# Optimization experiments

Hardware: AMD Instinct MI355X
Metric: run time of the kernel (lower is better)

Reference implementation:

```python
import jax, jax.numpy as jnp
import numpy as np

N = 262144      # number of 3D points
D = 128         # in_channels
NCLS = 20       # classes
M = 10          # num_prototype
EPS = 0.05      # sinkhorn epsilon
ITERS = 3       # sinkhorn iterations
GAMMA = 0.99    # EMA momentum
LN_EPS = 1e-5

def layer_norm(x, g, b):
    mu = jnp.mean(x, axis=-1, keepdims=True)
    v = jnp.mean((x - mu) ** 2, axis=-1, keepdims=True)
    return (x - mu) / jnp.sqrt(v + LN_EPS) * g + b

def l2n(x):
    # F.normalize(p=2, dim=-1) with eps=1e-12
    return x / jnp.clip(jnp.linalg.norm(x, axis=-1, keepdims=True), 1e-12)

def setup_inputs() -> dict:
    key = jax.random.key(0)
    k1, k2, k3 = jax.random.split(key, 3)
    return {
        "feature3d": jax.random.normal(k1, (N, D), dtype=jnp.float32),
        "gt_seg": jax.random.randint(k2, (N,), 0, NCLS, dtype=jnp.int32),
        "prototypes": jax.random.normal(k3, (NCLS, M, D), dtype=jnp.float32),
        "feat_gamma": jnp.ones((D,), jnp.float32),
        "feat_beta": jnp.zeros((D,), jnp.float32),
        "mask_gamma": jnp.ones((NCLS,), jnp.float32),
        "mask_beta": jnp.zeros((NCLS,), jnp.float32),
    }

def reference(feature3d, gt_seg, prototypes, feat_gamma, feat_beta, mask_gamma, mask_beta):
    _c = l2n(layer_norm(feature3d, feat_gamma, feat_beta))            # [N,D]
    protos = l2n(prototypes)                                          # [K,M,D]
    masks = jnp.einsum('nd,kmd->nmk', _c, protos)                     # [N,M,K]
    out_seg = layer_norm(jnp.max(masks, axis=1), mask_gamma, mask_beta)  # [N,K]

    # ---- prototype_learning ----
    pred = jnp.argmax(out_seg, axis=-1)
    correct = (gt_seg == pred).astype(_c.dtype)                       # [N]
    proto_logits = _c @ protos.reshape(-1, D).T                       # [N,K*M]

    sel = jax.nn.one_hot(gt_seg, NCLS, dtype=_c.dtype)                # [N,K]
    # masked per-class sinkhorn, vectorized across all 20 classes
    L = jnp.exp(jnp.transpose(masks, (2, 1, 0)) / EPS) * sel.T[:, None, :]  # [K,M,N]
    B = jnp.sum(sel, axis=0)                                          # [K] points per class
    s = jnp.sum(L, axis=(1, 2), keepdims=True)
    L = L / jnp.where(s > 0, s, 1.0)
    Bsafe = jnp.where(B > 0, B, 1.0)[:, None, None]
    for _ in range(ITERS):
        rs = jnp.sum(L, axis=2, keepdims=True)                        # per-prototype row sum
        L = L / (jnp.where(rs > 0, rs, 1.0) * M)
        cs = jnp.sum(L, axis=1, keepdims=True)                        # per-point col sum
        L = L / jnp.where(cs > 0, cs, 1.0) / Bsafe
    L = L * B[:, None, None]

    idx = jnp.argmax(L, axis=1)                                       # [K,N] hard assignment
    q = jax.nn.one_hot(idx, M, dtype=_c.dtype)                        # [K,N,M] (one_hot(argmax))

    w = sel.T * correct[None, :]                                      # [K,N] class-k AND correct
    m_q = q * w[:, :, None]                                           # [K,N,M]
    f = jnp.einsum('knm,nd->kmd', m_q, _c * correct[:, None])         # [K,M,D]
    ncount = jnp.sum(m_q, axis=1)                                     # [K,M]
    fn = l2n(f)
    upd = GAMMA * protos + (1.0 - GAMMA) * fn                         # momentum_update
    new_protos = l2n(jnp.where(ncount[..., None] > 0, upd, protos))   # [K,M,D]

    idx_pp = idx[gt_seg, jnp.arange(N)]                               # per-point proto index
    proto_target = (idx_pp + M * gt_seg).astype(jnp.float32)          # [N]
    return out_seg, proto_logits, proto_target, new_protos
```

## Files before the change

kernel.cpp:

```cpp
#include <hip/hip_runtime.h>
#include <hip/hip_bf16.h>

#define NPTS 262144
#define DIM  128
#define KC   20
#define MP   10
#define LNEPS 1e-5f
#define EPSI  0.05f
#define CCAP  65536

typedef _Float16 half8 __attribute__((ext_vector_type(8)));
typedef float f32x4 __attribute__((ext_vector_type(4)));

union H8U4 { half8 h; uint4 u; };

#define WS_PN     0
#define WS_PHI    25600
#define WS_PLO    39936
#define WS_F      54272
#define WS_NCOUNT 79872
#define WS_CCNT   80072
#define WS_UH     80080
#define WS_SK     80680
#define WS_BC     80700
#define WS_PSB    80720
#define WS_PR     244560
#define WS_EXPV   449360
#define WS_CIDX   3595088

#define MFMA_(b_, a_, c_) __builtin_amdgcn_mfma_f32_16x16x32_f16(b_, a_, c_, 0, 0, 0)

__device__ __forceinline__ half8 lds_h8(const uint4* p) {
    return *reinterpret_cast<const half8*>(p);
}

__device__ __forceinline__ void gload_lds16(const uint4* g, uint4* l) {
    __builtin_amdgcn_global_load_lds(
        (const __attribute__((address_space(1))) void*)(g),
        (__attribute__((address_space(3))) void*)(l), 16, 0, 0);
}

__global__ __launch_bounds__(64) void k_norm_protos(
    const float* __restrict__ pr, float* __restrict__ pn,
    _Float16* __restrict__ phi, _Float16* __restrict__ plo)
{
    int j = blockIdx.x, l = threadIdx.x;
    const int jm = j & 15;
    const int s1 = l >> 3,       swz1 = (((s1 ^ jm) << 3) | (l & 7));
    const int s2 = 8 + (l >> 3), swz2 = (((s2 ^ jm) << 3) | (l & 7));
    if (j < 200) {
        float x0 = pr[(size_t)j*128 + l], x1 = pr[(size_t)j*128 + 64 + l];
        float ss = x0*x0 + x1*x1;
        #pragma unroll
        for (int off = 32; off > 0; off >>= 1) ss += __shfl_xor(ss, off);
        float dn = fmaxf(sqrtf(ss), 1e-12f);
        float y0 = x0/dn, y1 = x1/dn;
        pn[(size_t)j*128 + l]      = y0;
        pn[(size_t)j*128 + 64 + l] = y1;
        _Float16 h0 = (_Float16)y0, h1 = (_Float16)y1;
        phi[(size_t)j*128 + swz1] = h0;
        phi[(size_t)j*128 + swz2] = h1;
        plo[(size_t)j*128 + swz1] = (_Float16)(y0 - (float)h0);
        plo[(size_t)j*128 + swz2] = (_Float16)(y1 - (float)h1);
    } else {
        phi[(size_t)j*128 + swz1] = (_Float16)0.f;  phi[(size_t)j*128 + swz2] = (_Float16)0.f;
        plo[(size_t)j*128 + swz1] = (_Float16)0.f;  plo[(size_t)j*128 + swz2] = (_Float16)0.f;
    }
}

__global__ __launch_bounds__(256, 3) void k_main(
    const float* __restrict__ feat, const int* __restrict__ gt,
    const _Float16* __restrict__ phi, const _Float16* __restrict__ plo,
    const float* __restrict__ fg, const float* __restrict__ fb,
    const float* __restrict__ mg, const float* __restrict__ mb,
    float* __restrict__ out_seg, float* __restrict__ plog,
    float* __restrict__ expv, float* __restrict__ psb,
    int* __restrict__ cidx, int* __restrict__ ccnt)
{
    __shared__ __align__(16) char ldsb[49152];
    __shared__ float sumS[64];
    __shared__ int   gtS[64];
    __shared__ float part[320];
    uint4* bbuf = (uint4*)ldsb;
    float* epi  = (float*)ldsb;

    const int t = threadIdx.x, blk = blockIdx.x;
    const int w = t >> 6, lane = t & 63;
    const int l15 = lane & 15, l4 = lane >> 4;
    const int pbase = blk * 64;

    const uint4* phi4 = (const uint4*)phi;
    const uint4* plo4 = (const uint4*)plo;

#define STAGE_B(S, BI) do { \
        const uint4* gh = phi4 + (size_t)(S)*512 + t; \
        const uint4* gl = plo4 + (size_t)(S)*512 + t; \
        uint4* dh = bbuf + (BI)*1024 + w*64; \
        uint4* dl = bbuf + (BI)*1024 + 512 + w*64; \
        gload_lds16(gh,       dh); \
        gload_lds16(gh + 256, dh + 256); \
        gload_lds16(gl,       dl); \
        gload_lds16(gl + 256, dl + 256); \
    } while (0)

    STAGE_B(0, 0);
    STAGE_B(1, 1);

    const float4* gfeat = (const float4*)feat;
    float4 A[4][2];
    {
        size_t rb = (size_t)(pbase + w*16 + l15) * 32;
        #pragma unroll
        for (int kst = 0; kst < 4; ++kst)
            #pragma unroll
            for (int h = 0; h < 2; ++h)
                A[kst][h] = gfeat[rb + kst*8 + l4*2 + h];
    }
    float4 G[4][2], Bb[4][2];
    {
        const float4* fg4 = (const float4*)fg;
        const float4* fb4 = (const float4*)fb;
        #pragma unroll
        for (int kst = 0; kst < 4; ++kst)
            #pragma unroll
            for (int h = 0; h < 2; ++h) {
                G[kst][h]  = fg4[kst*8 + l4*2 + h];
                Bb[kst][h] = fb4[kst*8 + l4*2 + h];
            }
    }

    half8 fah[4], fal[4];
    {
        float s0 = 0.f;
        #pragma unroll
        for (int kst = 0; kst < 4; ++kst)
            #pragma unroll
            for (int h = 0; h < 2; ++h) {
                float4 v = A[kst][h];
                s0 += v.x + v.y + v.z + v.w;
            }
        s0 += __shfl_xor(s0, 16); s0 += __shfl_xor(s0, 32);
        float mean = s0 * (1.f/128.f);
        float s1 = 0.f;
        #pragma unroll
        for (int kst = 0; kst < 4; ++kst)
            #pragma unroll
            for (int h = 0; h < 2; ++h) {
                float4 v = A[kst][h];
                float a = v.x-mean, b = v.y-mean, c = v.z-mean, d = v.w-mean;
                s1 += a*a + b*b + c*c + d*d;
            }
        s1 += __shfl_xor(s1, 16); s1 += __shfl_xor(s1, 32);
        float rstd = rsqrtf(s1 * (1.f/128.f) + LNEPS);
        float s2 = 0.f;
        #pragma unroll
        for (int kst = 0; kst < 4; ++kst)
            #pragma unroll
            for (int h = 0; h < 2; ++h) {
                float4 v = A[kst][h];
                float4 g = G[kst][h], bb = Bb[kst][h];
                v.x = (v.x-mean)*rstd*g.x + bb.x;
                v.y = (v.y-mean)*rstd*g.y + bb.y;
                v.z = (v.z-mean)*rstd*g.z + bb.z;
                v.w = (v.w-mean)*rstd*g.w + bb.w;
                A[kst][h] = v;
                s2 += v.x*v.x + v.y*v.y + v.z*v.z + v.w*v.w;
            }
        s2 += __shfl_xor(s2, 16); s2 += __shfl_xor(s2, 32);
        float rl2 = 1.f / fmaxf(sqrtf(s2), 1e-12f);
        #pragma unroll
        for (int kst = 0; kst < 4; ++kst) {
            float4 va = A[kst][0], vb = A[kst][1];
            va.x*=rl2; va.y*=rl2; va.z*=rl2; va.w*=rl2;
            vb.x*=rl2; vb.y*=rl2; vb.z*=rl2; vb.w*=rl2;
            H8U4 h, lo;
            h.h[0]=(_Float16)va.x; h.h[1]=(_Float16)va.y; h.h[2]=(_Float16)va.z; h.h[3]=(_Float16)va.w;
            h.h[4]=(_Float16)vb.x; h.h[5]=(_Float16)vb.y; h.h[6]=(_Float16)vb.z; h.h[7]=(_Float16)vb.w;
            lo.h[0]=(_Float16)(va.x-(float)h.h[0]); lo.h[1]=(_Float16)(va.y-(float)h.h[1]);
            lo.h[2]=(_Float16)(va.z-(float)h.h[2]); lo.h[3]=(_Float16)(va.w-(float)h.h[3]);
            lo.h[4]=(_Float16)(vb.x-(float)h.h[4]); lo.h[5]=(_Float16)(vb.y-(float)h.h[5]);
            lo.h[6]=(_Float16)(vb.z-(float)h.h[6]); lo.h[7]=(_Float16)(vb.w-(float)h.h[7]);
            fah[kst] = h.h;
            fal[kst] = lo.h;
        }
    }

    f32x4 acc[13];
    #pragma unroll
    for (int nt = 0; nt < 13; ++nt)
        acc[nt] = (f32x4){0.f,0.f,0.f,0.f};

    __syncthreads();

    #pragma unroll
    for (int s = 0; s < 7; ++s) {
        if (s < 5) STAGE_B(s + 2, (s + 2) % 3);
        const uint4* bb = bbuf + (s % 3)*1024;
        if (s < 6) {
            #pragma unroll
            for (int kst = 0; kst < 4; ++kst) {
                const int slz = (kst*4 + l4) ^ l15;
                half8 b0h = lds_h8(bb + l15*16 + slz);
                half8 b0l = lds_h8(bb + 512 + l15*16 + slz);
                half8 b1h = lds_h8(bb + (16+l15)*16 + slz);
                half8 b1l = lds_h8(bb + 512 + (16+l15)*16 + slz);
                acc[2*s]   = MFMA_(b0h, fah[kst], acc[2*s]);
                acc[2*s+1] = MFMA_(b1h, fah[kst], acc[2*s+1]);
                acc[2*s]   = MFMA_(b0h, fal[kst], acc[2*s]);
                acc[2*s+1] = MFMA_(b1h, fal[kst], acc[2*s+1]);
                acc[2*s]   = MFMA_(b0l, fah[kst], acc[2*s]);
                acc[2*s+1] = MFMA_(b1l, fah[kst], acc[2*s+1]);
                acc[2*s]   = MFMA_(b0l, fal[kst], acc[2*s]);
                acc[2*s+1] = MFMA_(b1l, fal[kst], acc[2*s+1]);
            }
        } else {
            #pragma unroll
            for (int kst = 0; kst < 4; ++kst) {
                const int slz = (kst*4 + l4) ^ l15;
                half8 b0h = lds_h8(bb + l15*16 + slz);
                half8 b0l = lds_h8(bb + 512 + l15*16 + slz);
                acc[12] = MFMA_(b0h, fah[kst], acc[12]);
                acc[12] = MFMA_(b0h, fal[kst], acc[12]);
                acc[12] = MFMA_(b0l, fah[kst], acc[12]);
                acc[12] = MFMA_(b0l, fal[kst], acc[12]);
            }
        }
        __syncthreads();
    }

    #pragma unroll 1
    for (int p = 0; p < 2; ++p) {
        if ((w >> 1) == p) {
            int row = (w & 1)*16 + l15;
            #pragma unroll
            for (int nt = 0; nt < 13; ++nt)
                if (nt < 12 || l4 < 2) {
                    float4 sv;
                    sv.x = acc[nt][0]; sv.y = acc[nt][1];
                    sv.z = acc[nt][2]; sv.w = acc[nt][3];
                    *reinterpret_cast<float4*>(&epi[row*210 + nt*16 + l4*4]) = sv;
                }
        }
        __syncthreads();
        if (t < 128) {
            const int q = t >> 2, sub = t & 3;
            const int n = pbase + p*32 + q;
            float ml[5];
            #pragma unroll
            for (int kk = 0; kk < 5; ++kk) {
                int k = sub*5 + kk;
                float mx = epi[q*210 + k*10];
                #pragma unroll
                for (int m = 1; m < 10; ++m) mx = fmaxf(mx, epi[q*210 + k*10 + m]);
                ml[kk] = mx;
            }
            float s0 = ml[0]+ml[1]+ml[2]+ml[3]+ml[4];
            s0 += __shfl_xor(s0,1); s0 += __shfl_xor(s0,2);
            float mean = s0 / 20.f;
            float s1 = 0.f;
            #pragma unroll
            for (int kk = 0; kk < 5; ++kk) { float d = ml[kk]-mean; s1 += d*d; }
            s1 += __shfl_xor(s1,1); s1 += __shfl_xor(s1,2);
            float rstd = rsqrtf(s1 / 20.f + LNEPS);
            float bv = -1e30f; int bk = 0;
            #pragma unroll
            for (int kk = 0; kk < 5; ++kk) {
                int k = sub*5 + kk;
                float y = (ml[kk]-mean)*rstd*mg[k] + mb[k];
                out_seg[(size_t)n*20 + k] = y;
                if (y > bv) { bv = y; bk = k; }
            }
            #pragma unroll
            for (int off = 1; off <= 2; off <<= 1) {
                float ov = __shfl_xor(bv, off);
                int   ok = __shfl_xor(bk, off);
                if (ov > bv || (ov == bv && ok < bk)) { bv = ov; bk = ok; }
            }
            int g = gt[n];
            if (sub == 0) {
                if (bk == g) {
                    int slot = atomicAdd(ccnt, 1);
                    if (slot < CCAP) cidx[slot] = n;
                }
                float se = 0.f;
                #pragma unroll
                for (int m = 0; m < 10; ++m) {
                    float e = expf(epi[q*210 + g*10 + m] / EPSI);
                    expv[(size_t)n*12 + m] = e;
                    se += e;
                }
                sumS[p*32 + q] = se;
                gtS[p*32 + q]  = g;
            }
        }
        __syncthreads();
    }

    if (t < 160) {
        int c = t >> 3, o = t & 7;
        float cnt = 0.f, sm = 0.f;
        for (int i = o*8; i < o*8 + 8; ++i)
            if (gtS[i] == c) { cnt += 1.f; sm += sumS[i]; }
        part[t] = cnt; part[160 + t] = sm;
    }
    __syncthreads();
    if (t < 20) {
        float cnt = 0.f, sm = 0.f;
        #pragma unroll
        for (int o = 0; o < 8; ++o) { cnt += part[t*8+o]; sm += part[160 + t*8+o]; }
        psb[(size_t)t*4096 + blk]      = cnt;
        psb[(size_t)(20+t)*4096 + blk] = sm;
    }

    #pragma unroll
    for (int nt = 0; nt < 13; ++nt)
        if (nt < 12 || l4 < 2) {
            float4 sv;
            sv.x = acc[nt][0]; sv.y = acc[nt][1];
            sv.z = acc[nt][2]; sv.w = acc[nt][3];
            *reinterpret_cast<float4*>(
                &plog[(size_t)(pbase + w*16 + l15)*200 + nt*16 + l4*4]) = sv;
        }
#undef STAGE_B
}

__global__ __launch_bounds__(256) void k_reduce_sB(
    const float* __restrict__ psb, float* __restrict__ sk, float* __restrict__ Bc)
{
    __shared__ float red[256];
    int t = threadIdx.x, rrow = blockIdx.x;
    float s = 0.f;
    #pragma unroll
    for (int i = 0; i < 16; ++i) s += psb[(size_t)rrow*4096 + i*256 + t];
    red[t] = s; __syncthreads();
    for (int off = 128; off > 0; off >>= 1) { if (t < off) red[t] += red[t+off]; __syncthreads(); }
    if (t == 0) { if (rrow < 20) Bc[rrow] = red[0]; else sk[rrow-20] = red[0]; }
}

__global__ __launch_bounds__(256) void k_row(int iter,
    const int* __restrict__ gt, const float* __restrict__ expv,
    const float* __restrict__ uh, const float* __restrict__ sk,
    const float* __restrict__ Bc, float* __restrict__ pr)
{
    __shared__ float prodS[2560];
    __shared__ int gtS[256];
    int t = threadIdx.x, b = blockIdx.x;
    int n = b*256 + t;
    int g = gt[n];
    float e[10];
    {
        const float4* e4 = (const float4*)(expv + (size_t)n*12);
        float4 ea = e4[0], eb = e4[1], ec = e4[2];
        e[0]=ea.x; e[1]=ea.y; e[2]=ea.z; e[3]=ea.w;
        e[4]=eb.x; e[5]=eb.y; e[6]=eb.z; e[7]=eb.w;
        e[8]=ec.x; e[9]=ec.y;
    }
    float skg = sk[g];
    float v = (skg > 0.f) ? 1.f/skg : 1.f;
    float B = Bc[g];
    float Bs = (B > 0.f) ? B : 1.f;
    for (int c = 1; c < iter; ++c) {
        const float* uc = uh + (c-1)*200 + g*10;
        float sc = 0.f;
        #pragma unroll
        for (int m = 0; m < 10; ++m) sc += e[m]*uc[m];
        v = (sc > 0.f) ? 1.f/(Bs*sc) : v/Bs;
    }
    #pragma unroll
    for (int m = 0; m < 10; ++m) prodS[t*10+m] = e[m]*v;
    gtS[t] = g;
    __syncthreads();
    if (t < 200) {
        int kk = t / 10, mm = t % 10;
        float acc = 0.f;
        for (int i = 0; i < 256; ++i)
            if (gtS[i] == kk) acc += prodS[i*10+mm];
        pr[(size_t)t*1024 + b] = acc;
    }
}

__global__ __launch_bounds__(256) void k_reduce_u(int iter,
    const float* __restrict__ pr, float* __restrict__ uh)
{
    __shared__ float red[256];
    int t = threadIdx.x, j = blockIdx.x;
    float s = 0.f;
    #pragma unroll
    for (int i = 0; i < 4; ++i) s += pr[(size_t)j*1024 + i*256 + t];
    red[t] = s; __syncthreads();
    for (int off = 128; off > 0; off >>= 1) { if (t < off) red[t] += red[t+off]; __syncthreads(); }
    if (t == 0) {
        float S = red[0];
        float uprev = (iter == 1) ? 1.f : uh[(iter-2)*200 + j];
        uh[(iter-1)*200 + j] = (S > 0.f) ? 1.f/(10.f*S) : uprev*0.1f;
    }
}

__global__ __launch_bounds__(256) void k_post(
    const int* __restrict__ gt, const float* __restrict__ expv,
    const float* __restrict__ u,
    const int* __restrict__ cidx, const int* __restrict__ ccnt,
    const float* __restrict__ feat, const float* __restrict__ fg,
    const float* __restrict__ fb,
    float* __restrict__ ptarget, float* __restrict__ facc,
    float* __restrict__ ncount)
{
    int t = threadIdx.x;
    {
        int n = blockIdx.x*256 + t;
        int g = gt[n];
        const float* uk = u + g*10;
        float bv = -1e30f; int idx = 0;
        #pragma unroll
        for (int m = 0; m < 10; ++m) {
            float pm = expv[(size_t)n*12 + m] * uk[m];
            if (pm > bv) { bv = pm; idx = m; }
        }
        ptarget[n] = (float)(idx + 10*g);
    }
    int wid = blockIdx.x*4 + (t >> 6);
    int lane = t & 63;
    int cnt = *ccnt; if (cnt > CCAP) cnt = CCAP;
    for (int i = wid; i < cnt; i += 4096) {
        int n = cidx[i];
        float x0 = feat[(size_t)n*128 + lane], x1 = feat[(size_t)n*128 + 64 + lane];
        float s = x0 + x1;
        #pragma unroll
        for (int off = 32; off > 0; off >>= 1) s += __shfl_xor(s, off);
        float mean = s * (1.f/128.f);
        float d0 = x0 - mean, d1 = x1 - mean;
        float s2 = d0*d0 + d1*d1;
        #pragma unroll
        for (int off = 32; off > 0; off >>= 1) s2 += __shfl_xor(s2, off);
        float rstd = rsqrtf(s2 * (1.f/128.f) + LNEPS);
        float y0 = d0*rstd*fg[lane] + fb[lane];
        float y1 = d1*rstd*fg[64+lane] + fb[64+lane];
        float s3 = y0*y0 + y1*y1;
        #pragma unroll
        for (int off = 32; off > 0; off >>= 1) s3 += __shfl_xor(s3, off);
        float rl2 = 1.f / fmaxf(sqrtf(s3), 1e-12f);
        float c0 = y0*rl2, c1 = y1*rl2;
        int g = gt[n];
        const float* uk = u + g*10;
        float bv = -1e30f; int idx = 0;
        #pragma unroll
        for (int m = 0; m < 10; ++m) {
            float pm = expv[(size_t)n*12 + m] * uk[m];
            if (pm > bv) { bv = pm; idx = m; }
        }
        float* frow = facc + (size_t)(g*10+idx)*128;
        atomicAdd(&frow[lane], c0);
        atomicAdd(&frow[64+lane], c1);
        if (lane == 0) atomicAdd(&ncount[g*10+idx], 1.f);
    }
}

__global__ __launch_bounds__(64) void k_proto_update(
    const float* __restrict__ facc, const float* __restrict__ ncount,
    const float* __restrict__ pn, float* __restrict__ outp)
{
    const float OMG = (float)(1.0 - 0.99);
    int j = blockIdx.x, l = threadIdx.x;
    float f0 = facc[(size_t)j*128+l], f1 = facc[(size_t)j*128+64+l];
    float ss = f0*f0 + f1*f1;
    #pragma unroll
    for (int off = 32; off > 0; off >>= 1) ss += __shfl_xor(ss, off);
    float fl2 = fmaxf(sqrtf(ss), 1e-12f);
    float fn0 = f0/fl2, fn1 = f1/fl2;
    float p0 = pn[(size_t)j*128+l], p1 = pn[(size_t)j*128+64+l];
    float u0 = 0.99f*p0 + OMG*fn0, u1 = 0.99f*p1 + OMG*fn1;
    bool ok = ncount[j] > 0.f;
    float s0 = ok ? u0 : p0, s1 = ok ? u1 : p1;
    float ss2 = s0*s0 + s1*s1;
    #pragma unroll
    for (int off = 32; off > 0; off >>= 1) ss2 += __shfl_xor(ss2, off);
    float l2 = fmaxf(sqrtf(ss2), 1e-12f);
    outp[(size_t)j*128+l]      = s0/l2;
    outp[(size_t)j*128+64+l]   = s1/l2;
}

extern "C" void kernel_launch(void* const* d_in, const int* in_sizes, int n_in,
                              void* d_out, int out_size, void* d_ws, size_t ws_size,
                              hipStream_t stream)
{
    const float* feat   = (const float*)d_in[0];
    const int*   gt     = (const int*)  d_in[1];
    const float* protos = (const float*)d_in[2];
    const float* fg     = (const float*)d_in[3];
    const float* fb     = (const float*)d_in[4];
    const float* mg     = (const float*)d_in[5];
    const float* mb     = (const float*)d_in[6];

    float* out      = (float*)d_out;
    float* out_seg  = out;
    float* plog     = out + (size_t)NPTS*20;
    float* ptarget  = out + (size_t)NPTS*220;
    float* newp     = out + (size_t)NPTS*221;

    float* ws   = (float*)d_ws;
    float* pn   = ws + WS_PN;
    _Float16* phi = (_Float16*)(ws + WS_PHI);
    _Float16* plo = (_Float16*)(ws + WS_PLO);
    float* facc = ws + WS_F;
    float* ncnt = ws + WS_NCOUNT;
    int*   ccnt = (int*)(ws + WS_CCNT);
    float* uh   = ws + WS_UH;
    float* sk   = ws + WS_SK;
    float* Bc   = ws + WS_BC;
    float* psb  = ws + WS_PSB;
    float* pr   = ws + WS_PR;
    float* expv = ws + WS_EXPV;
    int*   cidx = (int*)(ws + WS_CIDX);

    hipMemsetAsync(facc, 0, (25600 + 200 + 8)*sizeof(float), stream);
    hipLaunchKernelGGL(k_norm_protos, dim3(224), dim3(64), 0, stream, protos, pn, phi, plo);
    hipLaunchKernelGGL(k_main, dim3(4096), dim3(256), 0, stream,
                       feat, gt, phi, plo, fg, fb, mg, mb, out_seg, plog, expv, psb,
                       cidx, ccnt);
    hipLaunchKernelGGL(k_reduce_sB, dim3(40), dim3(256), 0, stream, psb, sk, Bc);
    for (int it = 1; it <= 3; ++it) {
        hipLaunchKernelGGL(k_row, dim3(1024), dim3(256), 0, stream, it, gt, expv, uh, sk, Bc, pr);
        hipLaunchKernelGGL(k_reduce_u, dim3(200), dim3(256), 0, stream, it, pr, uh);
    }
    hipLaunchKernelGGL(k_post, dim3(1024), dim3(256), 0, stream,
                       gt, expv, uh + 400, cidx, ccnt, feat, fg, fb, ptarget, facc, ncnt);
    hipLaunchKernelGGL(k_proto_update, dim3(200), dim3(64), 0, stream, facc, ncnt, pn, newp);
}
```

Measured before the change: 270.2 us.

## Coalesce k_main output stores via LDS and fuse Sinkhorn reductions into row kernels

```diff
diff --git a/kernel.cpp b/kernel.cpp
--- a/kernel.cpp
+++ b/kernel.cpp
@@ -28,6 +28,8 @@
 #define WS_EXPV   449360
 #define WS_CIDX   3595088
 
+#define EPIT 212
+
 #define MFMA_(b_, a_, c_) __builtin_amdgcn_mfma_f32_16x16x32_f16(b_, a_, c_, 0, 0, 0)
 
 __device__ __forceinline__ half8 lds_h8(const uint4* p) {
@@ -83,6 +85,8 @@
     __shared__ float part[320];
     uint4* bbuf = (uint4*)ldsb;
     float* epi  = (float*)ldsb;
+    float* osg  = (float*)(ldsb + 28672);
+    float* exs  = (float*)(ldsb + 31232);
 
     const int t = threadIdx.x, blk = blockIdx.x;
     const int w = t >> 6, lane = t & 63;
@@ -238,10 +242,22 @@
                     float4 sv;
                     sv.x = acc[nt][0]; sv.y = acc[nt][1];
                     sv.z = acc[nt][2]; sv.w = acc[nt][3];
-                    *reinterpret_cast<float4*>(&epi[row*210 + nt*16 + l4*4]) = sv;
+                    *reinterpret_cast<float4*>(&epi[row*EPIT + nt*16 + l4*4]) = sv;
                 }
         }
         __syncthreads();
+        {
+            float* pdst = plog + (size_t)(pbase + p*32)*200;
+            #pragma unroll
+            for (int it = 0; it < 7; ++it) {
+                int f = it*256 + t;
+                if (f < 1600) {
+                    int row = f / 50, c4 = f - row*50;
+                    float4 v = *reinterpret_cast<const float4*>(&epi[row*EPIT + c4*4]);
+                    *reinterpret_cast<float4*>(&pdst[(size_t)f*4]) = v;
+                }
+            }
+        }
         if (t < 128) {
             const int q = t >> 2, sub = t & 3;
             const int n = pbase + p*32 + q;
@@ -249,9 +265,9 @@
             #pragma unroll
             for (int kk = 0; kk < 5; ++kk) {
                 int k = sub*5 + kk;
-                float mx = epi[q*210 + k*10];
+                float mx = epi[q*EPIT + k*10];
                 #pragma unroll
-                for (int m = 1; m < 10; ++m) mx = fmaxf(mx, epi[q*210 + k*10 + m]);
+                for (int m = 1; m < 10; ++m) mx = fmaxf(mx, epi[q*EPIT + k*10 + m]);
                 ml[kk] = mx;
             }
             float s0 = ml[0]+ml[1]+ml[2]+ml[3]+ml[4];
@@ -267,7 +283,7 @@
             for (int kk = 0; kk < 5; ++kk) {
                 int k = sub*5 + kk;
                 float y = (ml[kk]-mean)*rstd*mg[k] + mb[k];
-                out_seg[(size_t)n*20 + k] = y;
+                osg[q*20 + k] = y;
                 if (y > bv) { bv = y; bk = k; }
             }
             #pragma unroll
@@ -285,14 +301,23 @@
                 float se = 0.f;
                 #pragma unroll
                 for (int m = 0; m < 10; ++m) {
-                    float e = expf(epi[q*210 + g*10 + m] / EPSI);
-                    expv[(size_t)n*12 + m] = e;
+                    float e = expf(epi[q*EPIT + g*10 + m] / EPSI);
+                    exs[q*12 + m] = e;
                     se += e;
                 }
+                exs[q*12 + 10] = 0.f;
+                exs[q*12 + 11] = 0.f;
                 sumS[p*32 + q] = se;
                 gtS[p*32 + q]  = g;
             }
         }
+        __syncthreads();
+        if (t < 160)
+            *reinterpret_cast<float4*>(&out_seg[(size_t)(pbase + p*32)*20 + t*4])
+                = *reinterpret_cast<const float4*>(&osg[t*4]);
+        else if (t < 256 && (t - 160) < 96)
+            *reinterpret_cast<float4*>(&expv[(size_t)(pbase + p*32)*12 + (t-160)*4])
+                = *reinterpret_cast<const float4*>(&exs[(t-160)*4]);
         __syncthreads();
     }
 
@@ -311,16 +336,6 @@
         psb[(size_t)t*4096 + blk]      = cnt;
         psb[(size_t)(20+t)*4096 + blk] = sm;
     }
-
-    #pragma unroll
-    for (int nt = 0; nt < 13; ++nt)
-        if (nt < 12 || l4 < 2) {
-            float4 sv;
-            sv.x = acc[nt][0]; sv.y = acc[nt][1];
-            sv.z = acc[nt][2]; sv.w = acc[nt][3];
-            *reinterpret_cast<float4*>(
-                &plog[(size_t)(pbase + w*16 + l15)*200 + nt*16 + l4*4]) = sv;
-        }
 #undef STAGE_B
 }
 
@@ -339,77 +354,98 @@
 
 __global__ __launch_bounds__(256) void k_row(int iter,
     const int* __restrict__ gt, const float* __restrict__ expv,
-    const float* __restrict__ uh, const float* __restrict__ sk,
-    const float* __restrict__ Bc, float* __restrict__ pr)
+    float* __restrict__ uh, const float* __restrict__ sk,
+    const float* __restrict__ Bc,
+    const float* __restrict__ prPrev, float* __restrict__ prCur)
 {
     __shared__ float prodS[2560];
     __shared__ int gtS[256];
+    __shared__ float uS[200];
+    __shared__ float u0S[200];
     int t = threadIdx.x, b = blockIdx.x;
-    int n = b*256 + t;
-    int g = gt[n];
-    float e[10];
-    {
-        const float4* e4 = (const float4*)(expv + (size_t)n*12);
-        float4 ea = e4[0], eb = e4[1], ec = e4[2];
-        e[0]=ea.x; e[1]=ea.y; e[2]=ea.z; e[3]=ea.w;
-        e[4]=eb.x; e[5]=eb.y; e[6]=eb.z; e[7]=eb.w;
-        e[8]=ec.x; e[9]=ec.y;
-    }
-    float skg = sk[g];
-    float v = (skg > 0.f) ? 1.f/skg : 1.f;
-    float B = Bc[g];
-    float Bs = (B > 0.f) ? B : 1.f;
-    for (int c = 1; c < iter; ++c) {
-        const float* uc = uh + (c-1)*200 + g*10;
-        float sc = 0.f;
-        #pragma unroll
-        for (int m = 0; m < 10; ++m) sc += e[m]*uc[m];
-        v = (sc > 0.f) ? 1.f/(Bs*sc) : v/Bs;
-    }
-    #pragma unroll
-    for (int m = 0; m < 10; ++m) prodS[t*10+m] = e[m]*v;
-    gtS[t] = g;
-    __syncthreads();
-    if (t < 200) {
-        int kk = t / 10, mm = t % 10;
-        float acc = 0.f;
-        for (int i = 0; i < 256; ++i)
-            if (gtS[i] == kk) acc += prodS[i*10+mm];
-        pr[(size_t)t*1024 + b] = acc;
-    }
-}
-
-__global__ __launch_bounds__(256) void k_reduce_u(int iter,
-    const float* __restrict__ pr, float* __restrict__ uh)
-{
-    __shared__ float red[256];
-    int t = threadIdx.x, j = blockIdx.x;
-    float s = 0.f;
-    #pragma unroll
-    for (int i = 0; i < 4; ++i) s += pr[(size_t)j*1024 + i*256 + t];
-    red[t] = s; __syncthreads();
-    for (int off = 128; off > 0; off >>= 1) { if (t < off) red[t] += red[t+off]; __syncthreads(); }
-    if (t == 0) {
-        float S = red[0];
-        float uprev = (iter == 1) ? 1.f : uh[(iter-2)*200 + j];
-        uh[(iter-1)*200 + j] = (S > 0.f) ? 1.f/(10.f*S) : uprev*0.1f;
-    }
+
+    if (iter > 1) {
+        if (t < 200) {
+            float s = 0.f;
+            for (int bb = 0; bb < 256; ++bb) s += prPrev[bb*224 + t];
+            float uprev = (iter == 2) ? 1.f : uh[(iter-3)*200 + t];
+            float val = (s > 0.f) ? 1.f/(10.f*s) : uprev*0.1f;
+            uS[t] = val;
+            if (b == 0) uh[(iter-2)*200 + t] = val;
+        }
+        if (iter == 3 && t < 200) u0S[t] = uh[t];
+    }
+
+    float acc = 0.f;
+    #pragma unroll 1
+    for (int ch = 0; ch < 4; ++ch) {
+        int n = (ch*256 + b)*256 + t;
+        int g = gt[n];
+        float e[10];
+        {
+            const float4* e4 = (const float4*)(expv + (size_t)n*12);
+            float4 ea = e4[0], eb = e4[1], ec = e4[2];
+            e[0]=ea.x; e[1]=ea.y; e[2]=ea.z; e[3]=ea.w;
+            e[4]=eb.x; e[5]=eb.y; e[6]=eb.z; e[7]=eb.w;
+            e[8]=ec.x; e[9]=ec.y;
+        }
+        float skg = sk[g];
+        float v = (skg > 0.f) ? 1.f/skg : 1.f;
+        float B = Bc[g];
+        float Bs = (B > 0.f) ? B : 1.f;
+        __syncthreads();
+        if (iter >= 2) {
+            {
+                const float* uc = (iter == 2) ? &uS[g*10] : &u0S[g*10];
+                float sc = 0.f;
+                #pragma unroll
+                for (int m = 0; m < 10; ++m) sc += e[m]*uc[m];
+                v = (sc > 0.f) ? 1.f/(Bs*sc) : v/Bs;
+            }
+            if (iter == 3) {
+                const float* uc = &uS[g*10];
+                float sc = 0.f;
+                #pragma unroll
+                for (int m = 0; m < 10; ++m) sc += e[m]*uc[m];
+                v = (sc > 0.f) ? 1.f/(Bs*sc) : v/Bs;
+            }
+        }
+        #pragma unroll
+        for (int m = 0; m < 10; ++m) prodS[t*10+m] = e[m]*v;
+        gtS[t] = g;
+        __syncthreads();
+        if (t < 200) {
+            int kk = t / 10, mm = t % 10;
+            for (int i = 0; i < 256; ++i)
+                if (gtS[i] == kk) acc += prodS[i*10+mm];
+        }
+    }
+    if (t < 200) prCur[b*224 + t] = acc;
 }
 
 __global__ __launch_bounds__(256) void k_post(
     const int* __restrict__ gt, const float* __restrict__ expv,
-    const float* __restrict__ u,
+    const float* __restrict__ uh, const float* __restrict__ pr3,
     const int* __restrict__ cidx, const int* __restrict__ ccnt,
     const float* __restrict__ feat, const float* __restrict__ fg,
     const float* __restrict__ fb,
     float* __restrict__ ptarget, float* __restrict__ facc,
     float* __restrict__ ncount)
 {
-    int t = threadIdx.x;
-    {
-        int n = blockIdx.x*256 + t;
+    __shared__ float uS[200];
+    int t = threadIdx.x, b = blockIdx.x;
+    if (t < 200) {
+        float s = 0.f;
+        for (int bb = 0; bb < 256; ++bb) s += pr3[bb*224 + t];
+        float uprev = uh[200 + t];
+        uS[t] = (s > 0.f) ? 1.f/(10.f*s) : uprev*0.1f;
+    }
+    __syncthreads();
+    #pragma unroll 1
+    for (int ch = 0; ch < 4; ++ch) {
+        int n = (ch*256 + b)*256 + t;
         int g = gt[n];
-        const float* uk = u + g*10;
+        const float* uk = &uS[g*10];
         float bv = -1e30f; int idx = 0;
         #pragma unroll
         for (int m = 0; m < 10; ++m) {
@@ -418,10 +454,10 @@
         }
         ptarget[n] = (float)(idx + 10*g);
     }
-    int wid = blockIdx.x*4 + (t >> 6);
+    int wid = b*4 + (t >> 6);
     int lane = t & 63;
     int cnt = *ccnt; if (cnt > CCAP) cnt = CCAP;
-    for (int i = wid; i < cnt; i += 4096) {
+    for (int i = wid; i < cnt; i += 1024) {
         int n = cidx[i];
         float x0 = feat[(size_t)n*128 + lane], x1 = feat[(size_t)n*128 + 64 + lane];
         float s = x0 + x1;
@@ -441,7 +477,7 @@
         float rl2 = 1.f / fmaxf(sqrtf(s3), 1e-12f);
         float c0 = y0*rl2, c1 = y1*rl2;
         int g = gt[n];
-        const float* uk = u + g*10;
+        const float* uk = &uS[g*10];
         float bv = -1e30f; int idx = 0;
         #pragma unroll
         for (int m = 0; m < 10; ++m) {
@@ -508,7 +544,9 @@
     float* sk   = ws + WS_SK;
     float* Bc   = ws + WS_BC;
     float* psb  = ws + WS_PSB;
-    float* pr   = ws + WS_PR;
+    float* pr1  = ws + WS_PR;
+    float* pr2  = ws + WS_PR + 57344;
+    float* pr3  = ws + WS_PR + 114688;
     float* expv = ws + WS_EXPV;
     int*   cidx = (int*)(ws + WS_CIDX);
 
@@ -518,11 +556,10 @@
                        feat, gt, phi, plo, fg, fb, mg, mb, out_seg, plog, expv, psb,
                        cidx, ccnt);
     hipLaunchKernelGGL(k_reduce_sB, dim3(40), dim3(256), 0, stream, psb, sk, Bc);
-    for (int it = 1; it <= 3; ++it) {
-        hipLaunchKernelGGL(k_row, dim3(1024), dim3(256), 0, stream, it, gt, expv, uh, sk, Bc, pr);
-        hipLaunchKernelGGL(k_reduce_u, dim3(200), dim3(256), 0, stream, it, pr, uh);
-    }
-    hipLaunchKernelGGL(k_post, dim3(1024), dim3(256), 0, stream,
-                       gt, expv, uh + 400, cidx, ccnt, feat, fg, fb, ptarget, facc, ncnt);
+    hipLaunchKernelGGL(k_row, dim3(256), dim3(256), 0, stream, 1, gt, expv, uh, sk, Bc, pr1, pr1);
+    hipLaunchKernelGGL(k_row, dim3(256), dim3(256), 0, stream, 2, gt, expv, uh, sk, Bc, pr1, pr2);
+    hipLaunchKernelGGL(k_row, dim3(256), dim3(256), 0, stream, 3, gt, expv, uh, sk, Bc, pr2, pr3);
+    hipLaunchKernelGGL(k_post, dim3(256), dim3(256), 0, stream,
+                       gt, expv, uh, pr3, cidx, ccnt, feat, fg, fb, ptarget, facc, ncnt);
     hipLaunchKernelGGL(k_proto_update, dim3(200), dim3(64), 0, stream, facc, ncnt, pn, newp);
 }
```

Measured after the change: 397.8 us. +47.2%, slower.
